# Performance work log

Hardware: AMD Instinct MI355X
Metric: run time of the kernel (lower is better)

The kernel has to match this reference:

```python
import jax, jax.numpy as jnp
import numpy as np


def setup_inputs() -> dict:
    key = jax.random.key(0)
    k1, k2 = jax.random.split(key)
    x = jax.random.normal(k1, (32, 64, 64, 64), dtype=jnp.float32)  # [B, C, H, W]
    limit = 3 ** 0.5
    embeddings = jax.random.uniform(k2, (64, 512), dtype=jnp.float32,
                                    minval=-limit, maxval=limit)  # [D, K]
    return {"x": x, "embeddings": embeddings}


def reference(x, embeddings):
    B, D, H, W = x.shape
    # NCHW -> NHWC -> [N, D]
    flat_x = jnp.transpose(x, (0, 2, 3, 1)).reshape(-1, D)
    distances = (
        jnp.sum(flat_x ** 2, axis=1, keepdims=True)
        - 2.0 * flat_x @ embeddings
        + jnp.sum(embeddings ** 2, axis=0, keepdims=True)
    )
    encoding_indices = jnp.argmin(distances, axis=1)  # [N]
    # gather codebook rows: embeddings.T is [K, D]
    quantized = embeddings.T[encoding_indices].reshape(B, H, W, D)
    quantized = jnp.transpose(quantized, (0, 3, 1, 2))  # back to NCHW
    commitment_loss = jnp.mean((x - jax.lax.stop_gradient(quantized)) ** 2)
    # straight-through estimator
    quantized_ste = x + jax.lax.stop_gradient(quantized - x)
    return quantized_ste, commitment_loss, encoding_indices.reshape(B, -1)
```

## Files before the change

kernel.cpp:

```cpp
#include <hip/hip_runtime.h>

#define D      64
#define K      512
#define Q_OFF  0
#define L_OFF  8388608
#define I_OFF  8388609

#define WS_ET    0
#define WS_EN    32768
#define WS_ENH   33280
#define WS_PART  33792

#define B_LO_OFF 4096

#define SEL_SCALE 16384.0f
#define SEL_BIAS  (160.0f * 16384.0f)

typedef __attribute__((ext_vector_type(8))) short short8;
typedef __attribute__((ext_vector_type(4))) float f32x4;

static __device__ __forceinline__ unsigned short f2bf(float f) {
    unsigned u = __float_as_uint(f);
    u += 0x7fffu + ((u >> 16) & 1u);
    return (unsigned short)(u >> 16);
}
static __device__ __forceinline__ float bf2f(unsigned short h) {
    return __uint_as_float(((unsigned)h) << 16);
}

__device__ __forceinline__ void gload_lds16(const float* g, float* l) {
    __builtin_amdgcn_global_load_lds(
        (const __attribute__((address_space(1))) unsigned int*)g,
        (__attribute__((address_space(3))) unsigned int*)l, 16, 0, 0);
}

__global__ __launch_bounds__(256) void vq_prep(const float* __restrict__ E,
                                               float* __restrict__ ws,
                                               float* __restrict__ out) {
    int g = blockIdx.x * 256 + threadIdx.x;
    int t = g >> 6, lane = g & 63;
    int col = lane & 15, kg = lane >> 4;
    int code = t * 16 + col;
    short8* bhp = (short8*)out;
    short8* blp = (short8*)out + B_LO_OFF;
#pragma unroll
    for (int s = 0; s < 2; ++s) {
        short8 h, l;
#pragma unroll
        for (int j = 0; j < 8; ++j) {
            int k = s * 32 + kg * 8 + j;
            float v = -E[k * K + code];
            unsigned short hb = f2bf(v);
            h[j] = (short)hb;
            l[j] = (short)f2bf(v - bf2f(hb));
        }
        bhp[(t * 2 + s) * 64 + lane] = h;
        blp[(t * 2 + s) * 64 + lane] = l;
    }
    if (g < K) {
        float nsq = 0.f;
#pragma unroll 8
        for (int d = 0; d < D; ++d) {
            float v = E[d * K + g];
            ws[WS_ET + g * D + d] = v;
            nsq = fmaf(v, v, nsq);
        }
        ws[WS_EN + g]  = nsq;
        ws[WS_ENH + g] = 0.5f * nsq;
    }
}

__global__ __launch_bounds__(128, 4) void vq_dist(const float* __restrict__ x,
                                                  const float* __restrict__ ws,
                                                  float* __restrict__ out) {
    __shared__ float sbuf[2][2048];
    __shared__ float senh[512];

    const int tid = threadIdx.x, w = tid >> 6, lane = tid & 63;
    const int col = lane & 15, rowg = lane >> 4;
    const int pixw = blockIdx.x * 64 + w * 32;

    const float* bh  = (const float*)out;
    const float* bl  = (const float*)out + B_LO_OFF * 4;

    {
        float* db = sbuf[0];
#pragma unroll
        for (int q = 0; q < 2; ++q) {
            gload_lds16(bh + q * 512 + tid * 4, db + q * 512 + tid * 4);
            gload_lds16(bl + q * 512 + tid * 4, db + 1024 + q * 512 + tid * 4);
        }
        gload_lds16(ws + WS_ENH + tid * 4, senh + tid * 4);
    }

    short8 ah[2][2], al[2][2];
#pragma unroll
    for (int mt = 0; mt < 2; ++mt) {
        int pix = pixw + mt * 16 + col;
        const float* xp = x + ((size_t)(pix >> 12) << 18) + (pix & 4095);
#pragma unroll
        for (int s = 0; s < 2; ++s) {
            short8 h, l;
#pragma unroll
            for (int j = 0; j < 8; ++j) {
                float v = xp[(size_t)(s * 32 + rowg * 8 + j) << 12];
                unsigned short hb = f2bf(v);
                h[j] = (short)hb;
                l[j] = (short)f2bf(v - bf2f(hb));
            }
            ah[mt][s] = h; al[mt][s] = l;
        }
    }

    unsigned m1[2][4], m2[2][4];
#pragma unroll
    for (int mt = 0; mt < 2; ++mt)
#pragma unroll
        for (int r = 0; r < 4; ++r) { m1[mt][r] = 0xFFFFFFFFu; m2[mt][r] = 0xFFFFFFFFu; }

    __syncthreads();

#pragma unroll 2
    for (int c = 0; c < 16; ++c) {
        if (c + 1 < 16) {
            const float* sh = bh + (c + 1) * 1024;
            const float* sl = bl + (c + 1) * 1024;
            float* db = sbuf[(c + 1) & 1];
#pragma unroll
            for (int q = 0; q < 2; ++q) {
                gload_lds16(sh + q * 512 + tid * 4, db + q * 512 + tid * 4);
                gload_lds16(sl + q * 512 + tid * 4, db + 1024 + q * 512 + tid * 4);
            }
        }

        const short8* sb = (const short8*)sbuf[c & 1];
#pragma unroll
        for (int p = 0; p < 2; ++p) {
            const int t = c * 2 + p;
            const float ev = senh[t * 16 + col];
            const unsigned codev = (unsigned)(t * 16 + col);

            short8 cbh0 = sb[p * 128 + lane];
            short8 cbh1 = sb[p * 128 + 64 + lane];
            short8 cbl0 = sb[256 + p * 128 + lane];
            short8 cbl1 = sb[256 + p * 128 + 64 + lane];

            f32x4 acc0 = { ev, ev, ev, ev };
            f32x4 acc1 = { ev, ev, ev, ev };
            __builtin_amdgcn_s_setprio(1);
            acc0 = __builtin_amdgcn_mfma_f32_16x16x32_bf16(ah[0][0], cbh0, acc0, 0, 0, 0);
            acc0 = __builtin_amdgcn_mfma_f32_16x16x32_bf16(al[0][0], cbh0, acc0, 0, 0, 0);
            acc0 = __builtin_amdgcn_mfma_f32_16x16x32_bf16(ah[0][0], cbl0, acc0, 0, 0, 0);
            acc0 = __builtin_amdgcn_mfma_f32_16x16x32_bf16(ah[0][1], cbh1, acc0, 0, 0, 0);
            acc0 = __builtin_amdgcn_mfma_f32_16x16x32_bf16(al[0][1], cbh1, acc0, 0, 0, 0);
            acc0 = __builtin_amdgcn_mfma_f32_16x16x32_bf16(ah[0][1], cbl1, acc0, 0, 0, 0);
            acc1 = __builtin_amdgcn_mfma_f32_16x16x32_bf16(ah[1][0], cbh0, acc1, 0, 0, 0);
            acc1 = __builtin_amdgcn_mfma_f32_16x16x32_bf16(al[1][0], cbh0, acc1, 0, 0, 0);
            acc1 = __builtin_amdgcn_mfma_f32_16x16x32_bf16(ah[1][0], cbl0, acc1, 0, 0, 0);
            acc1 = __builtin_amdgcn_mfma_f32_16x16x32_bf16(ah[1][1], cbh1, acc1, 0, 0, 0);
            acc1 = __builtin_amdgcn_mfma_f32_16x16x32_bf16(al[1][1], cbh1, acc1, 0, 0, 0);
            acc1 = __builtin_amdgcn_mfma_f32_16x16x32_bf16(ah[1][1], cbl1, acc1, 0, 0, 0);
            __builtin_amdgcn_s_setprio(0);

#pragma unroll
            for (int r = 0; r < 4; ++r) {
                unsigned u0 = (unsigned)fmaf(acc0[r], SEL_SCALE, SEL_BIAS);
                unsigned p0 = (u0 << 9) + codev;
                m2[0][r] = min(m2[0][r], max(m1[0][r], p0));
                m1[0][r] = min(m1[0][r], p0);
                unsigned u1 = (unsigned)fmaf(acc1[r], SEL_SCALE, SEL_BIAS);
                unsigned p1 = (u1 << 9) + codev;
                m2[1][r] = min(m2[1][r], max(m1[1][r], p1));
                m1[1][r] = min(m1[1][r], p1);
            }
        }
        __syncthreads();
    }

    unsigned* outu = (unsigned*)out;
#pragma unroll
    for (int mt = 0; mt < 2; ++mt)
#pragma unroll
        for (int r = 0; r < 4; ++r) {
            unsigned v1 = m1[mt][r], v2 = m2[mt][r];
#pragma unroll
            for (int m = 1; m < 16; m <<= 1) {
                unsigned o1 = (unsigned)__shfl_xor((int)v1, m, 16);
                unsigned o2 = (unsigned)__shfl_xor((int)v2, m, 16);
                v2 = min(max(v1, o1), min(v2, o2));
                v1 = min(v1, o1);
            }
            if (col == r) {
                int p = pixw + mt * 16 + rowg * 4 + r;
                unsigned c1 = v1 & 511u, c2 = v2 & 511u;
                outu[I_OFF + p] = c1 | (c2 << 16);
            }
        }
}

__device__ __forceinline__ float dotrow(const float* __restrict__ er,
                                        const float* __restrict__ xv) {
    const float4* e4 = (const float4*)er;
    float a0 = 0.f, a1 = 0.f, a2 = 0.f, a3 = 0.f;
#pragma unroll
    for (int q = 0; q < 16; ++q) {
        float4 e = e4[q];
        a0 = fmaf(xv[4*q+0], e.x, a0);
        a1 = fmaf(xv[4*q+1], e.y, a1);
        a2 = fmaf(xv[4*q+2], e.z, a2);
        a3 = fmaf(xv[4*q+3], e.w, a3);
    }
    return (a0 + a1) + (a2 + a3);
}

__global__ __launch_bounds__(256) void vq_out(const float* __restrict__ x,
                                              const float* __restrict__ ws,
                                              float* __restrict__ out,
                                              float* __restrict__ partial) {
    const float* ET = ws + WS_ET;
    const float* EN = ws + WS_EN;
    int n  = blockIdx.x * 256 + threadIdx.x;
    int b  = n >> 12;
    int hw = n & 4095;

    const float* xp = x + ((size_t)b << 18) + hw;
    float xv[D];
#pragma unroll
    for (int d = 0; d < D; ++d) xv[d] = xp[(size_t)d << 12];

    unsigned packed = ((const unsigned*)out)[I_OFF + n];
    int c1 = (int)(packed & 0xffffu), c2 = (int)(packed >> 16);

    float d1 = fmaf(-2.f, dotrow(ET + (c1 << 6), xv), EN[c1]);
    float d2 = fmaf(-2.f, dotrow(ET + (c2 << 6), xv), EN[c2]);
    bool sw = (d2 < d1) || (d2 == d1 && c2 < c1);
    int bestk = sw ? c2 : c1;

    out[I_OFF + n] = (float)bestk;

    const float* qv = ET + (bestk << 6);
    float* op = out + Q_OFF + ((size_t)b << 18) + hw;
    float lsum = 0.f;
#pragma unroll
    for (int d = 0; d < D; ++d) {
        float qd = qv[d];
        op[(size_t)d << 12] = qd;
        float diff = xv[d] - qd;
        lsum = fmaf(diff, diff, lsum);
    }

#pragma unroll
    for (int off = 32; off > 0; off >>= 1)
        lsum += __shfl_down(lsum, off, 64);
    __shared__ float wsum[4];
    if ((threadIdx.x & 63) == 0) wsum[threadIdx.x >> 6] = lsum;
    __syncthreads();
    if (threadIdx.x == 0)
        partial[blockIdx.x] = (wsum[0] + wsum[1]) + (wsum[2] + wsum[3]);
}

__global__ __launch_bounds__(256) void vq_final(const float* __restrict__ partial,
                                                float* __restrict__ out) {
    int t = threadIdx.x;
    float s = partial[t] + partial[t + 256];
#pragma unroll
    for (int off = 32; off > 0; off >>= 1)
        s += __shfl_down(s, off, 64);
    __shared__ float wsum[4];
    if ((t & 63) == 0) wsum[t >> 6] = s;
    __syncthreads();
    if (t == 0)
        out[L_OFF] = ((wsum[0] + wsum[1]) + (wsum[2] + wsum[3])) * (1.f / 8388608.f);
}

extern "C" void kernel_launch(void* const* d_in, const int* in_sizes, int n_in,
                              void* d_out, int out_size, void* d_ws, size_t ws_size,
                              hipStream_t stream) {
    const float* x = (const float*)d_in[0];
    const float* E = (const float*)d_in[1];
    float* out = (float*)d_out;
    float* ws  = (float*)d_ws;

    hipLaunchKernelGGL(vq_prep,  dim3(8),    dim3(256), 0, stream, E, ws, out);
    hipLaunchKernelGGL(vq_dist,  dim3(2048), dim3(128), 0, stream, x, ws, out);
    hipLaunchKernelGGL(vq_out,   dim3(512),  dim3(256), 0, stream, x, ws, out, ws + WS_PART);
    hipLaunchKernelGGL(vq_final, dim3(1),    dim3(256), 0, stream, ws + WS_PART, out);
}
```

Before: 66.85 us.

## Interleave MFMA chains in distance loop and split vq_out over channel halves

The distance kernel now processes both 16-code tiles of a chunk together, interleaving four independent MFMA accumulator chains and keeping separate top-2 trackers per tile, which are merged before the cross-lane reduction. The aim is to hide MFMA dependency latency, at the cost of more registers. The output kernel now splits each pixel's 64 channels across two thread halves. Each half computes partial dot products that are combined through shared memory, doubling the grid to 1024 blocks for more parallelism and fewer registers per thread. The final reduction reads 1024 partial sums to match.

Result: slower. 68.63 us (+2.7%).

```diff
diff --git a/kernel.cpp b/kernel.cpp
--- a/kernel.cpp
+++ b/kernel.cpp
@@ -112,15 +112,14 @@
         }
     }
 
-    unsigned m1[2][4], m2[2][4];
+    unsigned m1[2][8], m2[2][8];
 #pragma unroll
     for (int mt = 0; mt < 2; ++mt)
 #pragma unroll
-        for (int r = 0; r < 4; ++r) { m1[mt][r] = 0xFFFFFFFFu; m2[mt][r] = 0xFFFFFFFFu; }
+        for (int r = 0; r < 8; ++r) { m1[mt][r] = 0xFFFFFFFFu; m2[mt][r] = 0xFFFFFFFFu; }
 
     __syncthreads();
 
-#pragma unroll 2
     for (int c = 0; c < 16; ++c) {
         if (c + 1 < 16) {
             const float* sh = bh + (c + 1) * 1024;
@@ -134,45 +133,62 @@
         }
 
         const short8* sb = (const short8*)sbuf[c & 1];
-#pragma unroll
-        for (int p = 0; p < 2; ++p) {
-            const int t = c * 2 + p;
-            const float ev = senh[t * 16 + col];
-            const unsigned codev = (unsigned)(t * 16 + col);
-
-            short8 cbh0 = sb[p * 128 + lane];
-            short8 cbh1 = sb[p * 128 + 64 + lane];
-            short8 cbl0 = sb[256 + p * 128 + lane];
-            short8 cbl1 = sb[256 + p * 128 + 64 + lane];
-
-            f32x4 acc0 = { ev, ev, ev, ev };
-            f32x4 acc1 = { ev, ev, ev, ev };
-            __builtin_amdgcn_s_setprio(1);
-            acc0 = __builtin_amdgcn_mfma_f32_16x16x32_bf16(ah[0][0], cbh0, acc0, 0, 0, 0);
-            acc0 = __builtin_amdgcn_mfma_f32_16x16x32_bf16(al[0][0], cbh0, acc0, 0, 0, 0);
-            acc0 = __builtin_amdgcn_mfma_f32_16x16x32_bf16(ah[0][0], cbl0, acc0, 0, 0, 0);
-            acc0 = __builtin_amdgcn_mfma_f32_16x16x32_bf16(ah[0][1], cbh1, acc0, 0, 0, 0);
-            acc0 = __builtin_amdgcn_mfma_f32_16x16x32_bf16(al[0][1], cbh1, acc0, 0, 0, 0);
-            acc0 = __builtin_amdgcn_mfma_f32_16x16x32_bf16(ah[0][1], cbl1, acc0, 0, 0, 0);
-            acc1 = __builtin_amdgcn_mfma_f32_16x16x32_bf16(ah[1][0], cbh0, acc1, 0, 0, 0);
-            acc1 = __builtin_amdgcn_mfma_f32_16x16x32_bf16(al[1][0], cbh0, acc1, 0, 0, 0);
-            acc1 = __builtin_amdgcn_mfma_f32_16x16x32_bf16(ah[1][0], cbl0, acc1, 0, 0, 0);
-            acc1 = __builtin_amdgcn_mfma_f32_16x16x32_bf16(ah[1][1], cbh1, acc1, 0, 0, 0);
-            acc1 = __builtin_amdgcn_mfma_f32_16x16x32_bf16(al[1][1], cbh1, acc1, 0, 0, 0);
-            acc1 = __builtin_amdgcn_mfma_f32_16x16x32_bf16(ah[1][1], cbl1, acc1, 0, 0, 0);
-            __builtin_amdgcn_s_setprio(0);
-
-#pragma unroll
-            for (int r = 0; r < 4; ++r) {
-                unsigned u0 = (unsigned)fmaf(acc0[r], SEL_SCALE, SEL_BIAS);
-                unsigned p0 = (u0 << 9) + codev;
-                m2[0][r] = min(m2[0][r], max(m1[0][r], p0));
-                m1[0][r] = min(m1[0][r], p0);
-                unsigned u1 = (unsigned)fmaf(acc1[r], SEL_SCALE, SEL_BIAS);
-                unsigned p1 = (u1 << 9) + codev;
-                m2[1][r] = min(m2[1][r], max(m1[1][r], p1));
-                m1[1][r] = min(m1[1][r], p1);
-            }
+        const float ev0 = senh[c * 32 + col];
+        const float ev1 = senh[c * 32 + 16 + col];
+
+        short8 bh0a = sb[lane],        bh1a = sb[64 + lane];
+        short8 bh0b = sb[128 + lane],  bh1b = sb[192 + lane];
+        short8 bl0a = sb[256 + lane],  bl1a = sb[320 + lane];
+        short8 bl0b = sb[384 + lane],  bl1b = sb[448 + lane];
+
+        f32x4 a00 = { ev0, ev0, ev0, ev0 };
+        f32x4 a01 = { ev1, ev1, ev1, ev1 };
+        f32x4 a10 = { ev0, ev0, ev0, ev0 };
+        f32x4 a11 = { ev1, ev1, ev1, ev1 };
+
+        __builtin_amdgcn_s_setprio(1);
+        a00 = __builtin_amdgcn_mfma_f32_16x16x32_bf16(ah[0][0], bh0a, a00, 0, 0, 0);
+        a01 = __builtin_amdgcn_mfma_f32_16x16x32_bf16(ah[0][0], bh0b, a01, 0, 0, 0);
+        a10 = __builtin_amdgcn_mfma_f32_16x16x32_bf16(ah[1][0], bh0a, a10, 0, 0, 0);
+        a11 = __builtin_amdgcn_mfma_f32_16x16x32_bf16(ah[1][0], bh0b, a11, 0, 0, 0);
+        a00 = __builtin_amdgcn_mfma_f32_16x16x32_bf16(al[0][0], bh0a, a00, 0, 0, 0);
+        a01 = __builtin_amdgcn_mfma_f32_16x16x32_bf16(al[0][0], bh0b, a01, 0, 0, 0);
+        a10 = __builtin_amdgcn_mfma_f32_16x16x32_bf16(al[1][0], bh0a, a10, 0, 0, 0);
+        a11 = __builtin_amdgcn_mfma_f32_16x16x32_bf16(al[1][0], bh0b, a11, 0, 0, 0);
+        a00 = __builtin_amdgcn_mfma_f32_16x16x32_bf16(ah[0][0], bl0a, a00, 0, 0, 0);
+        a01 = __builtin_amdgcn_mfma_f32_16x16x32_bf16(ah[0][0], bl0b, a01, 0, 0, 0);
+        a10 = __builtin_amdgcn_mfma_f32_16x16x32_bf16(ah[1][0], bl0a, a10, 0, 0, 0);
+        a11 = __builtin_amdgcn_mfma_f32_16x16x32_bf16(ah[1][0], bl0b, a11, 0, 0, 0);
+        a00 = __builtin_amdgcn_mfma_f32_16x16x32_bf16(ah[0][1], bh1a, a00, 0, 0, 0);
+        a01 = __builtin_amdgcn_mfma_f32_16x16x32_bf16(ah[0][1], bh1b, a01, 0, 0, 0);
+        a10 = __builtin_amdgcn_mfma_f32_16x16x32_bf16(ah[1][1], bh1a, a10, 0, 0, 0);
+        a11 = __builtin_amdgcn_mfma_f32_16x16x32_bf16(ah[1][1], bh1b, a11, 0, 0, 0);
+        a00 = __builtin_amdgcn_mfma_f32_16x16x32_bf16(al[0][1], bh1a, a00, 0, 0, 0);
+        a01 = __builtin_amdgcn_mfma_f32_16x16x32_bf16(al[0][1], bh1b, a01, 0, 0, 0);
+        a10 = __builtin_amdgcn_mfma_f32_16x16x32_bf16(al[1][1], bh1a, a10, 0, 0, 0);
+        a11 = __builtin_amdgcn_mfma_f32_16x16x32_bf16(al[1][1], bh1b, a11, 0, 0, 0);
+        a00 = __builtin_amdgcn_mfma_f32_16x16x32_bf16(ah[0][1], bl1a, a00, 0, 0, 0);
+        a01 = __builtin_amdgcn_mfma_f32_16x16x32_bf16(ah[0][1], bl1b, a01, 0, 0, 0);
+        a10 = __builtin_amdgcn_mfma_f32_16x16x32_bf16(ah[1][1], bl1a, a10, 0, 0, 0);
+        a11 = __builtin_amdgcn_mfma_f32_16x16x32_bf16(ah[1][1], bl1b, a11, 0, 0, 0);
+        __builtin_amdgcn_s_setprio(0);
+
+        const unsigned cv0 = (unsigned)(c * 32 + col);
+        const unsigned cv1 = (unsigned)(c * 32 + 16 + col);
+#pragma unroll
+        for (int r = 0; r < 4; ++r) {
+            unsigned p00 = (((unsigned)fmaf(a00[r], SEL_SCALE, SEL_BIAS)) << 9) + cv0;
+            m2[0][r] = min(m2[0][r], max(m1[0][r], p00));
+            m1[0][r] = min(m1[0][r], p00);
+            unsigned p01 = (((unsigned)fmaf(a01[r], SEL_SCALE, SEL_BIAS)) << 9) + cv1;
+            m2[0][4 + r] = min(m2[0][4 + r], max(m1[0][4 + r], p01));
+            m1[0][4 + r] = min(m1[0][4 + r], p01);
+            unsigned p10 = (((unsigned)fmaf(a10[r], SEL_SCALE, SEL_BIAS)) << 9) + cv0;
+            m2[1][r] = min(m2[1][r], max(m1[1][r], p10));
+            m1[1][r] = min(m1[1][r], p10);
+            unsigned p11 = (((unsigned)fmaf(a11[r], SEL_SCALE, SEL_BIAS)) << 9) + cv1;
+            m2[1][4 + r] = min(m2[1][4 + r], max(m1[1][4 + r], p11));
+            m1[1][4 + r] = min(m1[1][4 + r], p11);
         }
         __syncthreads();
     }
@@ -183,10 +199,13 @@
 #pragma unroll
         for (int r = 0; r < 4; ++r) {
             unsigned v1 = m1[mt][r], v2 = m2[mt][r];
+            unsigned o1 = m1[mt][4 + r], o2 = m2[mt][4 + r];
+            v2 = min(max(v1, o1), min(v2, o2));
+            v1 = min(v1, o1);
 #pragma unroll
             for (int m = 1; m < 16; m <<= 1) {
-                unsigned o1 = (unsigned)__shfl_xor((int)v1, m, 16);
-                unsigned o2 = (unsigned)__shfl_xor((int)v2, m, 16);
+                o1 = (unsigned)__shfl_xor((int)v1, m, 16);
+                o2 = (unsigned)__shfl_xor((int)v2, m, 16);
                 v2 = min(max(v1, o1), min(v2, o2));
                 v1 = min(v1, o1);
             }
@@ -198,12 +217,12 @@
         }
 }
 
-__device__ __forceinline__ float dotrow(const float* __restrict__ er,
-                                        const float* __restrict__ xv) {
+__device__ __forceinline__ float dot32(const float* __restrict__ er,
+                                       const float* __restrict__ xv) {
     const float4* e4 = (const float4*)er;
     float a0 = 0.f, a1 = 0.f, a2 = 0.f, a3 = 0.f;
 #pragma unroll
-    for (int q = 0; q < 16; ++q) {
+    for (int q = 0; q < 8; ++q) {
         float4 e = e4[q];
         a0 = fmaf(xv[4*q+0], e.x, a0);
         a1 = fmaf(xv[4*q+1], e.y, a1);
@@ -219,30 +238,40 @@
                                               float* __restrict__ partial) {
     const float* ET = ws + WS_ET;
     const float* EN = ws + WS_EN;
-    int n  = blockIdx.x * 256 + threadIdx.x;
-    int b  = n >> 12;
-    int hw = n & 4095;
-
-    const float* xp = x + ((size_t)b << 18) + hw;
-    float xv[D];
-#pragma unroll
-    for (int d = 0; d < D; ++d) xv[d] = xp[(size_t)d << 12];
+    const int tid  = threadIdx.x;
+    const int pl   = tid & 127;
+    const int half = tid >> 7;
+    const int n    = blockIdx.x * 128 + pl;
+    const int b    = n >> 12;
+    const int hw   = n & 4095;
+
+    const float* xp = x + ((size_t)b << 18) + ((size_t)half << 17) + hw;
+    float xv[32];
+#pragma unroll
+    for (int d = 0; d < 32; ++d) xv[d] = xp[(size_t)d << 12];
 
     unsigned packed = ((const unsigned*)out)[I_OFF + n];
     int c1 = (int)(packed & 0xffffu), c2 = (int)(packed >> 16);
 
-    float d1 = fmaf(-2.f, dotrow(ET + (c1 << 6), xv), EN[c1]);
-    float d2 = fmaf(-2.f, dotrow(ET + (c2 << 6), xv), EN[c2]);
+    float dp1 = dot32(ET + (c1 << 6) + half * 32, xv);
+    float dp2 = dot32(ET + (c2 << 6) + half * 32, xv);
+
+    __shared__ float2 sdot[2][128];
+    sdot[half][pl] = make_float2(dp1, dp2);
+    __syncthreads();
+    float2 lo = sdot[0][pl], hi = sdot[1][pl];
+    float d1 = fmaf(-2.f, lo.x + hi.x, EN[c1]);
+    float d2 = fmaf(-2.f, lo.y + hi.y, EN[c2]);
     bool sw = (d2 < d1) || (d2 == d1 && c2 < c1);
     int bestk = sw ? c2 : c1;
 
-    out[I_OFF + n] = (float)bestk;
-
-    const float* qv = ET + (bestk << 6);
-    float* op = out + Q_OFF + ((size_t)b << 18) + hw;
+    if (!half) out[I_OFF + n] = (float)bestk;
+
+    const float* qv = ET + (bestk << 6) + half * 32;
+    float* op = out + Q_OFF + ((size_t)b << 18) + ((size_t)half << 17) + hw;
     float lsum = 0.f;
 #pragma unroll
-    for (int d = 0; d < D; ++d) {
+    for (int d = 0; d < 32; ++d) {
         float qd = qv[d];
         op[(size_t)d << 12] = qd;
         float diff = xv[d] - qd;
@@ -253,16 +282,16 @@
     for (int off = 32; off > 0; off >>= 1)
         lsum += __shfl_down(lsum, off, 64);
     __shared__ float wsum[4];
-    if ((threadIdx.x & 63) == 0) wsum[threadIdx.x >> 6] = lsum;
+    if ((tid & 63) == 0) wsum[tid >> 6] = lsum;
     __syncthreads();
-    if (threadIdx.x == 0)
+    if (tid == 0)
         partial[blockIdx.x] = (wsum[0] + wsum[1]) + (wsum[2] + wsum[3]);
 }
 
 __global__ __launch_bounds__(256) void vq_final(const float* __restrict__ partial,
                                                 float* __restrict__ out) {
     int t = threadIdx.x;
-    float s = partial[t] + partial[t + 256];
+    float s = ((partial[t] + partial[t + 256]) + partial[t + 512]) + partial[t + 768];
 #pragma unroll
     for (int off = 32; off > 0; off >>= 1)
         s += __shfl_down(s, off, 64);
@@ -283,6 +312,6 @@
 
     hipLaunchKernelGGL(vq_prep,  dim3(8),    dim3(256), 0, stream, E, ws, out);
     hipLaunchKernelGGL(vq_dist,  dim3(2048), dim3(128), 0, stream, x, ws, out);
-    hipLaunchKernelGGL(vq_out,   dim3(512),  dim3(256), 0, stream, x, ws, out, ws + WS_PART);
+    hipLaunchKernelGGL(vq_out,   dim3(1024), dim3(256), 0, stream, x, ws, out, ws + WS_PART);
     hipLaunchKernelGGL(vq_final, dim3(1),    dim3(256), 0, stream, ws + WS_PART, out);
 }
```

## Triple-buffer codebook pipeline in vq_dist and split vq_out across channel halves

Applied to the files above, without the earlier changes.

vq_dist now streams the codebook in 32 smaller chunks through a three-slot LDS ring. It waits with an explicit vmcnt and a raw barrier instead of double-buffered __syncthreads, and it interleaves the two MFMA accumulator chains. The aim is to overlap global-to-LDS loads with compute and hide MFMA dependency latency. vq_out splits each pixel's 64 channels across two threads and doubles the grid to raise parallelism and reduce register pressure, combining the partial dot products through LDS. vq_final sums 1024 partials instead of 512. The hand-rolled waitcnt depends on the exact count of outstanding loads, which risks subtle races.

Result: slower. 69.45 us (+3.9%).

```diff
diff --git a/kernel.cpp b/kernel.cpp
--- a/kernel.cpp
+++ b/kernel.cpp
@@ -73,7 +73,7 @@
 __global__ __launch_bounds__(128, 4) void vq_dist(const float* __restrict__ x,
                                                   const float* __restrict__ ws,
                                                   float* __restrict__ out) {
-    __shared__ float sbuf[2][2048];
+    __shared__ float sbuf[3][1024];
     __shared__ float senh[512];
 
     const int tid = threadIdx.x, w = tid >> 6, lane = tid & 63;
@@ -84,13 +84,12 @@
     const float* bl  = (const float*)out + B_LO_OFF * 4;
 
     {
-        float* db = sbuf[0];
-#pragma unroll
-        for (int q = 0; q < 2; ++q) {
-            gload_lds16(bh + q * 512 + tid * 4, db + q * 512 + tid * 4);
-            gload_lds16(bl + q * 512 + tid * 4, db + 1024 + q * 512 + tid * 4);
-        }
-        gload_lds16(ws + WS_ENH + tid * 4, senh + tid * 4);
+#pragma unroll
+        for (int q = 0; q < 1; ++q) gload_lds16(ws + WS_ENH + tid * 4, senh + tid * 4);
+        gload_lds16(bh + tid * 4,       sbuf[0] + tid * 4);
+        gload_lds16(bl + tid * 4,       sbuf[0] + 512 + tid * 4);
+        gload_lds16(bh + 512 + tid * 4, sbuf[1] + tid * 4);
+        gload_lds16(bl + 512 + tid * 4, sbuf[1] + 512 + tid * 4);
     }
 
     short8 ah[2][2], al[2][2];
@@ -118,63 +117,57 @@
 #pragma unroll
         for (int r = 0; r < 4; ++r) { m1[mt][r] = 0xFFFFFFFFu; m2[mt][r] = 0xFFFFFFFFu; }
 
-    __syncthreads();
-
-#pragma unroll 2
-    for (int c = 0; c < 16; ++c) {
-        if (c + 1 < 16) {
-            const float* sh = bh + (c + 1) * 1024;
-            const float* sl = bl + (c + 1) * 1024;
-            float* db = sbuf[(c + 1) & 1];
-#pragma unroll
-            for (int q = 0; q < 2; ++q) {
-                gload_lds16(sh + q * 512 + tid * 4, db + q * 512 + tid * 4);
-                gload_lds16(sl + q * 512 + tid * 4, db + 1024 + q * 512 + tid * 4);
-            }
-        }
-
-        const short8* sb = (const short8*)sbuf[c & 1];
-#pragma unroll
-        for (int p = 0; p < 2; ++p) {
-            const int t = c * 2 + p;
-            const float ev = senh[t * 16 + col];
-            const unsigned codev = (unsigned)(t * 16 + col);
-
-            short8 cbh0 = sb[p * 128 + lane];
-            short8 cbh1 = sb[p * 128 + 64 + lane];
-            short8 cbl0 = sb[256 + p * 128 + lane];
-            short8 cbl1 = sb[256 + p * 128 + 64 + lane];
-
-            f32x4 acc0 = { ev, ev, ev, ev };
-            f32x4 acc1 = { ev, ev, ev, ev };
-            __builtin_amdgcn_s_setprio(1);
-            acc0 = __builtin_amdgcn_mfma_f32_16x16x32_bf16(ah[0][0], cbh0, acc0, 0, 0, 0);
-            acc0 = __builtin_amdgcn_mfma_f32_16x16x32_bf16(al[0][0], cbh0, acc0, 0, 0, 0);
-            acc0 = __builtin_amdgcn_mfma_f32_16x16x32_bf16(ah[0][0], cbl0, acc0, 0, 0, 0);
-            acc0 = __builtin_amdgcn_mfma_f32_16x16x32_bf16(ah[0][1], cbh1, acc0, 0, 0, 0);
-            acc0 = __builtin_amdgcn_mfma_f32_16x16x32_bf16(al[0][1], cbh1, acc0, 0, 0, 0);
-            acc0 = __builtin_amdgcn_mfma_f32_16x16x32_bf16(ah[0][1], cbl1, acc0, 0, 0, 0);
-            acc1 = __builtin_amdgcn_mfma_f32_16x16x32_bf16(ah[1][0], cbh0, acc1, 0, 0, 0);
-            acc1 = __builtin_amdgcn_mfma_f32_16x16x32_bf16(al[1][0], cbh0, acc1, 0, 0, 0);
-            acc1 = __builtin_amdgcn_mfma_f32_16x16x32_bf16(ah[1][0], cbl0, acc1, 0, 0, 0);
-            acc1 = __builtin_amdgcn_mfma_f32_16x16x32_bf16(ah[1][1], cbh1, acc1, 0, 0, 0);
-            acc1 = __builtin_amdgcn_mfma_f32_16x16x32_bf16(al[1][1], cbh1, acc1, 0, 0, 0);
-            acc1 = __builtin_amdgcn_mfma_f32_16x16x32_bf16(ah[1][1], cbl1, acc1, 0, 0, 0);
-            __builtin_amdgcn_s_setprio(0);
-
-#pragma unroll
-            for (int r = 0; r < 4; ++r) {
-                unsigned u0 = (unsigned)fmaf(acc0[r], SEL_SCALE, SEL_BIAS);
-                unsigned p0 = (u0 << 9) + codev;
-                m2[0][r] = min(m2[0][r], max(m1[0][r], p0));
-                m1[0][r] = min(m1[0][r], p0);
-                unsigned u1 = (unsigned)fmaf(acc1[r], SEL_SCALE, SEL_BIAS);
-                unsigned p1 = (u1 << 9) + codev;
-                m2[1][r] = min(m2[1][r], max(m1[1][r], p1));
-                m1[1][r] = min(m1[1][r], p1);
-            }
-        }
-        __syncthreads();
+    int cbuf = 0;
+    for (int c = 0; c < 32; ++c) {
+        asm volatile("s_waitcnt vmcnt(2)" ::: "memory");
+        __builtin_amdgcn_s_barrier();
+        __builtin_amdgcn_sched_barrier(0);
+
+        if (c + 2 < 32) {
+            int sb2 = (cbuf >= 1) ? cbuf - 1 : 2;
+            const float* sh = bh + (c + 2) * 512;
+            const float* sl = bl + (c + 2) * 512;
+            gload_lds16(sh + tid * 4, sbuf[sb2] + tid * 4);
+            gload_lds16(sl + tid * 4, sbuf[sb2] + 512 + tid * 4);
+        }
+
+        const short8* sb = (const short8*)sbuf[cbuf];
+        const float ev = senh[c * 16 + col];
+        const unsigned codev = (unsigned)(c * 16 + col);
+
+        short8 cbh0 = sb[lane];
+        short8 cbh1 = sb[64 + lane];
+        short8 cbl0 = sb[128 + lane];
+        short8 cbl1 = sb[192 + lane];
+
+        f32x4 acc0 = { ev, ev, ev, ev };
+        f32x4 acc1 = { ev, ev, ev, ev };
+        __builtin_amdgcn_s_setprio(1);
+        acc0 = __builtin_amdgcn_mfma_f32_16x16x32_bf16(ah[0][0], cbh0, acc0, 0, 0, 0);
+        acc1 = __builtin_amdgcn_mfma_f32_16x16x32_bf16(ah[1][0], cbh0, acc1, 0, 0, 0);
+        acc0 = __builtin_amdgcn_mfma_f32_16x16x32_bf16(al[0][0], cbh0, acc0, 0, 0, 0);
+        acc1 = __builtin_amdgcn_mfma_f32_16x16x32_bf16(al[1][0], cbh0, acc1, 0, 0, 0);
+        acc0 = __builtin_amdgcn_mfma_f32_16x16x32_bf16(ah[0][0], cbl0, acc0, 0, 0, 0);
+        acc1 = __builtin_amdgcn_mfma_f32_16x16x32_bf16(ah[1][0], cbl0, acc1, 0, 0, 0);
+        acc0 = __builtin_amdgcn_mfma_f32_16x16x32_bf16(ah[0][1], cbh1, acc0, 0, 0, 0);
+        acc1 = __builtin_amdgcn_mfma_f32_16x16x32_bf16(ah[1][1], cbh1, acc1, 0, 0, 0);
+        acc0 = __builtin_amdgcn_mfma_f32_16x16x32_bf16(al[0][1], cbh1, acc0, 0, 0, 0);
+        acc1 = __builtin_amdgcn_mfma_f32_16x16x32_bf16(al[1][1], cbh1, acc1, 0, 0, 0);
+        acc0 = __builtin_amdgcn_mfma_f32_16x16x32_bf16(ah[0][1], cbl1, acc0, 0, 0, 0);
+        acc1 = __builtin_amdgcn_mfma_f32_16x16x32_bf16(ah[1][1], cbl1, acc1, 0, 0, 0);
+        __builtin_amdgcn_s_setprio(0);
+
+#pragma unroll
+        for (int r = 0; r < 4; ++r) {
+            unsigned p0 = (((unsigned)fmaf(acc0[r], SEL_SCALE, SEL_BIAS)) << 9) + codev;
+            m2[0][r] = min(m2[0][r], max(m1[0][r], p0));
+            m1[0][r] = min(m1[0][r], p0);
+            unsigned p1 = (((unsigned)fmaf(acc1[r], SEL_SCALE, SEL_BIAS)) << 9) + codev;
+            m2[1][r] = min(m2[1][r], max(m1[1][r], p1));
+            m1[1][r] = min(m1[1][r], p1);
+        }
+
+        cbuf = (cbuf == 2) ? 0 : cbuf + 1;
     }
 
     unsigned* outu = (unsigned*)out;
@@ -198,12 +191,12 @@
         }
 }
 
-__device__ __forceinline__ float dotrow(const float* __restrict__ er,
-                                        const float* __restrict__ xv) {
+__device__ __forceinline__ float dot32(const float* __restrict__ er,
+                                       const float* __restrict__ xv) {
     const float4* e4 = (const float4*)er;
     float a0 = 0.f, a1 = 0.f, a2 = 0.f, a3 = 0.f;
 #pragma unroll
-    for (int q = 0; q < 16; ++q) {
+    for (int q = 0; q < 8; ++q) {
         float4 e = e4[q];
         a0 = fmaf(xv[4*q+0], e.x, a0);
         a1 = fmaf(xv[4*q+1], e.y, a1);
@@ -219,30 +212,40 @@
                                               float* __restrict__ partial) {
     const float* ET = ws + WS_ET;
     const float* EN = ws + WS_EN;
-    int n  = blockIdx.x * 256 + threadIdx.x;
-    int b  = n >> 12;
-    int hw = n & 4095;
-
-    const float* xp = x + ((size_t)b << 18) + hw;
-    float xv[D];
-#pragma unroll
-    for (int d = 0; d < D; ++d) xv[d] = xp[(size_t)d << 12];
+    const int tid  = threadIdx.x;
+    const int pl   = tid & 127;
+    const int half = tid >> 7;
+    const int n    = blockIdx.x * 128 + pl;
+    const int b    = n >> 12;
+    const int hw   = n & 4095;
+
+    const float* xp = x + ((size_t)b << 18) + ((size_t)half << 17) + hw;
+    float xv[32];
+#pragma unroll
+    for (int d = 0; d < 32; ++d) xv[d] = xp[(size_t)d << 12];
 
     unsigned packed = ((const unsigned*)out)[I_OFF + n];
     int c1 = (int)(packed & 0xffffu), c2 = (int)(packed >> 16);
 
-    float d1 = fmaf(-2.f, dotrow(ET + (c1 << 6), xv), EN[c1]);
-    float d2 = fmaf(-2.f, dotrow(ET + (c2 << 6), xv), EN[c2]);
+    float dp1 = dot32(ET + (c1 << 6) + half * 32, xv);
+    float dp2 = dot32(ET + (c2 << 6) + half * 32, xv);
+
+    __shared__ float2 sdot[2][128];
+    sdot[half][pl] = make_float2(dp1, dp2);
+    __syncthreads();
+    float2 lo = sdot[0][pl], hi = sdot[1][pl];
+    float d1 = fmaf(-2.f, lo.x + hi.x, EN[c1]);
+    float d2 = fmaf(-2.f, lo.y + hi.y, EN[c2]);
     bool sw = (d2 < d1) || (d2 == d1 && c2 < c1);
     int bestk = sw ? c2 : c1;
 
-    out[I_OFF + n] = (float)bestk;
-
-    const float* qv = ET + (bestk << 6);
-    float* op = out + Q_OFF + ((size_t)b << 18) + hw;
+    if (!half) out[I_OFF + n] = (float)bestk;
+
+    const float* qv = ET + (bestk << 6) + half * 32;
+    float* op = out + Q_OFF + ((size_t)b << 18) + ((size_t)half << 17) + hw;
     float lsum = 0.f;
 #pragma unroll
-    for (int d = 0; d < D; ++d) {
+    for (int d = 0; d < 32; ++d) {
         float qd = qv[d];
         op[(size_t)d << 12] = qd;
         float diff = xv[d] - qd;
@@ -253,16 +256,16 @@
     for (int off = 32; off > 0; off >>= 1)
         lsum += __shfl_down(lsum, off, 64);
     __shared__ float wsum[4];
-    if ((threadIdx.x & 63) == 0) wsum[threadIdx.x >> 6] = lsum;
+    if ((tid & 63) == 0) wsum[tid >> 6] = lsum;
     __syncthreads();
-    if (threadIdx.x == 0)
+    if (tid == 0)
         partial[blockIdx.x] = (wsum[0] + wsum[1]) + (wsum[2] + wsum[3]);
 }
 
 __global__ __launch_bounds__(256) void vq_final(const float* __restrict__ partial,
                                                 float* __restrict__ out) {
     int t = threadIdx.x;
-    float s = partial[t] + partial[t + 256];
+    float s = ((partial[t] + partial[t + 256]) + partial[t + 512]) + partial[t + 768];
 #pragma unroll
     for (int off = 32; off > 0; off >>= 1)
         s += __shfl_down(s, off, 64);
@@ -283,6 +286,6 @@
 
     hipLaunchKernelGGL(vq_prep,  dim3(8),    dim3(256), 0, stream, E, ws, out);
     hipLaunchKernelGGL(vq_dist,  dim3(2048), dim3(128), 0, stream, x, ws, out);
-    hipLaunchKernelGGL(vq_out,   dim3(512),  dim3(256), 0, stream, x, ws, out, ws + WS_PART);
+    hipLaunchKernelGGL(vq_out,   dim3(1024), dim3(256), 0, stream, x, ws, out, ws + WS_PART);
     hipLaunchKernelGGL(vq_final, dim3(1),    dim3(256), 0, stream, ws + WS_PART, out);
 }
```
